# Kernel tuning notes

Measured on AMD Instinct MI355X. Metric: run time of the kernel, lower is better.

## Reference

```python
import jax, jax.numpy as jnp
import numpy as np

NUM_ITERATIONS = 3


def squash(x, axis):
    # squared_norm/(1+squared_norm) * x / sqrt(squared_norm), as in the torch module
    sn = jnp.sum(x * x, axis=axis, keepdims=True)
    return sn / (1.0 + sn) * x / jnp.sqrt(sn)


def setup_inputs() -> dict:
    key = jax.random.key(0)
    k1, k2 = jax.random.split(key)
    batch, num_caps, num_route, in_ch, out_ch = 32, 32, 4608, 8, 16
    x = jax.random.normal(k1, (batch, num_route, in_ch), dtype=jnp.float32)
    route_weights = jax.random.normal(k2, (num_caps, num_route, in_ch, out_ch), dtype=jnp.float32)
    return {"x": x, "route_weights": route_weights}


def reference(x, route_weights):
    # U[b,c,r,1,o] = x[b,1,r,1,i] @ W[1,c,r,i,o]
    U = jnp.einsum("bri,crio->bcro", x, route_weights)[:, :, :, None, :]  # [b,c,r,1,o]
    B = jnp.zeros_like(U)
    V = None
    for _ in range(NUM_ITERATIONS):
        C = jax.nn.softmax(B, axis=1)                 # softmax over capsules
        S = jnp.sum(C * U, axis=2, keepdims=True)      # reduce over route nodes: [b,c,1,1,o]
        V = squash(S, axis=-1)
        B = B + U * V
    b, c = B.shape[0], B.shape[1]
    o = B.shape[-1]
    return V.reshape(b, c, o)
```

## Files before the change

kernel.cpp:

```cpp
#include <hip/hip_runtime.h>

#define BATCH 32
#define NCAPS 32
#define NR    4608
#define NI    8
#define NO    16
#define CSTR  200
#define MAXRB 36
#define L2E   1.44269504088896341f

typedef float f2 __attribute__((ext_vector_type(2)));

template<int RB, bool FIRST>
__global__ __launch_bounds__(1024, 2) void caps_route_fast(
    const float* __restrict__ x,
    const float* __restrict__ W,
    const float* __restrict__ A,
    float* __restrict__ P)
{
    __shared__ __align__(16) float Ws[2][NCAPS * CSTR];
    __shared__ __align__(16) f2    xP[RB][8][2][NI];

    const int t  = threadIdx.x;
    const int om = (t & 3) | (((t >> 3) & 1) << 2);
    const int co = ((t >> 4) & 1) | (((t >> 2) & 1) << 1) | (((t >> 5) & 1) << 2);
    const int w  = t >> 6;
    const int oh = w & 1;
    const int bq = w >> 1;
    const int o  = oh * 8 + om;
    const int b0 = 4 * bq;
    const int r0 = blockIdx.x * RB;

    f2 a2[2][4];
    if (!FIRST) {
#pragma unroll
        for (int p = 0; p < 2; ++p)
#pragma unroll
            for (int cl = 0; cl < 4; ++cl) {
                const int c = 4 * co + cl;
                a2[p][cl].x = A[((b0 + 2 * p + 0) * NCAPS + c) * NO + o] * L2E;
                a2[p][cl].y = A[((b0 + 2 * p + 1) * NCAPS + c) * NO + o] * L2E;
            }
    }
    f2 acc[2][4];
#pragma unroll
    for (int p = 0; p < 2; ++p)
#pragma unroll
        for (int cl = 0; cl < 4; ++cl) acc[p][cl] = (f2)0.f;

    for (int s = t; s < RB * 16; s += 1024) {
        const int rr = s >> 4, bp = s & 15;
        const float* xp0 = &x[((size_t)(2 * bp + 0) * NR + r0 + rr) * NI];
        const float* xp1 = &x[((size_t)(2 * bp + 1) * NR + r0 + rr) * NI];
        const float4 a0 = *(const float4*)xp0;
        const float4 a1 = *(const float4*)(xp0 + 4);
        const float4 c0 = *(const float4*)xp1;
        const float4 c1 = *(const float4*)(xp1 + 4);
        f2* d = &xP[rr][bp >> 1][bp & 1][0];
        d[0] = f2{a0.x, c0.x}; d[1] = f2{a0.y, c0.y};
        d[2] = f2{a0.z, c0.z}; d[3] = f2{a0.w, c0.w};
        d[4] = f2{a1.x, c1.x}; d[5] = f2{a1.y, c1.y};
        d[6] = f2{a1.z, c1.z}; d[7] = f2{a1.w, c1.w};
    }

    const int c_st = t >> 5;
    const int sl   = (c_st >> 2) + 8 * (c_st & 3);
    const int part = t & 31;
    const int i_st = part >> 2;
    const int o0   = (part & 3) * 4;
    const float* wsrc = W + ((size_t)c_st * NR + r0) * (NI * NO) + part * 4;

    {
        const float4 s0 = *(const float4*)wsrc;
        float* d = &Ws[0][sl * CSTR + o0 * 12 + i_st];
        d[0] = s0.x; d[12] = s0.y; d[24] = s0.z; d[36] = s0.w;
    }
    float4 pf = {};
    if (RB > 1) pf = *(const float4*)(wsrc + NI * NO);
    __syncthreads();

#pragma unroll 1
    for (int rr = 0; rr < RB; ++rr) {
        const int cur = rr & 1;

        if (rr + 1 < RB) {
            float* d = &Ws[cur ^ 1][sl * CSTR + o0 * 12 + i_st];
            d[0] = pf.x; d[12] = pf.y; d[24] = pf.z; d[36] = pf.w;
            if (rr + 2 < RB)
                pf = *(const float4*)(wsrc + (size_t)(rr + 2) * (NI * NO));
        }

        f2 xq[2][NI];
        {
            const f2* xv = &xP[rr][bq][0][0];
#pragma unroll
            for (int i = 0; i < NI; ++i) { xq[0][i] = xv[i]; xq[1][i] = xv[NI + i]; }
        }

        const float* wb = &Ws[cur][co * CSTR + o * 12];
        if (FIRST) {
#pragma unroll
            for (int cl = 0; cl < 4; ++cl) {
                const float* wp = wb + cl * (8 * CSTR);
                const float4 w0 = *(const float4*)wp;
                const float4 w1 = *(const float4*)(wp + 4);
#pragma unroll
                for (int p = 0; p < 2; ++p) {
                    f2 u2 = xq[p][0] * w0.x;
                    u2 += xq[p][1] * w0.y;
                    u2 += xq[p][2] * w0.z;
                    u2 += xq[p][3] * w0.w;
                    u2 += xq[p][4] * w1.x;
                    u2 += xq[p][5] * w1.y;
                    u2 += xq[p][6] * w1.z;
                    u2 += xq[p][7] * w1.w;
                    acc[p][cl] += u2;
                }
            }
        } else {
            f2 tt[2][4];
            f2 Z0 = (f2)0.f, Z1 = (f2)0.f;
#pragma unroll
            for (int cl = 0; cl < 4; ++cl) {
                const float* wp = wb + cl * (8 * CSTR);
                const float4 w0 = *(const float4*)wp;
                const float4 w1 = *(const float4*)(wp + 4);
                f2 u0 = xq[0][0] * w0.x;
                u0 += xq[0][1] * w0.y;
                u0 += xq[0][2] * w0.z;
                u0 += xq[0][3] * w0.w;
                u0 += xq[0][4] * w1.x;
                u0 += xq[0][5] * w1.y;
                u0 += xq[0][6] * w1.z;
                u0 += xq[0][7] * w1.w;
                f2 u1 = xq[1][0] * w0.x;
                u1 += xq[1][1] * w0.y;
                u1 += xq[1][2] * w0.z;
                u1 += xq[1][3] * w0.w;
                u1 += xq[1][4] * w1.x;
                u1 += xq[1][5] * w1.y;
                u1 += xq[1][6] * w1.z;
                u1 += xq[1][7] * w1.w;
                const f2 l0 = u0 * a2[0][cl];
                const f2 l1 = u1 * a2[1][cl];
                f2 e0, e1;
                e0.x = exp2f(l0.x); e0.y = exp2f(l0.y);
                e1.x = exp2f(l1.x); e1.y = exp2f(l1.y);
                Z0 += e0; Z1 += e1;
                tt[0][cl] = e0 * u0;
                tt[1][cl] = e1 * u1;
            }
#pragma unroll
            for (int m = 0; m < 3; ++m) {
                const int msk = (m == 0) ? 4 : (m == 1) ? 16 : 32;
                Z0.x += __shfl_xor(Z0.x, msk); Z0.y += __shfl_xor(Z0.y, msk);
                Z1.x += __shfl_xor(Z1.x, msk); Z1.y += __shfl_xor(Z1.y, msk);
            }
            f2 rz0, rz1;
            rz0.x = __builtin_amdgcn_rcpf(Z0.x); rz0.y = __builtin_amdgcn_rcpf(Z0.y);
            rz1.x = __builtin_amdgcn_rcpf(Z1.x); rz1.y = __builtin_amdgcn_rcpf(Z1.y);
#pragma unroll
            for (int cl = 0; cl < 4; ++cl) {
                acc[0][cl] += tt[0][cl] * rz0;
                acc[1][cl] += tt[1][cl] * rz1;
            }
        }
        __syncthreads();
    }

#pragma unroll
    for (int bb = 0; bb < 4; ++bb) {
        const int p = bb >> 1, h = bb & 1;
        float* pout = P + (((size_t)blockIdx.x * BATCH + b0 + bb) * NO + o) * NCAPS + 4 * co;
        float4 v;
        v.x = h ? acc[p][0].y : acc[p][0].x;
        v.y = h ? acc[p][1].y : acc[p][1].x;
        v.z = h ? acc[p][2].y : acc[p][2].x;
        v.w = h ? acc[p][3].y : acc[p][3].x;
        if (FIRST) { v.x *= 0.03125f; v.y *= 0.03125f; v.z *= 0.03125f; v.w *= 0.03125f; }
        *(float4*)pout = v;
    }
}

__global__ __launch_bounds__(256) void caps_partial(const float* __restrict__ P,
                                                    float* __restrict__ P2)
{
    const int tid = threadIdx.x;
    const int ct  = blockIdx.x & 15;
    const int rg  = blockIdx.x >> 4;
    const size_t col = (size_t)ct * 1024 + tid * 4;
    const float* p = P + (size_t)rg * 16 * 16384 + col;
    float4 s = {0.f, 0.f, 0.f, 0.f};
#pragma unroll
    for (int k = 0; k < 16; ++k) {
        const float4 v = *(const float4*)(p + (size_t)k * 16384);
        s.x += v.x; s.y += v.y; s.z += v.z; s.w += v.w;
    }
    *(float4*)(P2 + (size_t)rg * 16384 + col) = s;
}

__global__ void caps_reduce_squash(const float* __restrict__ P,
                                   float* __restrict__ A,
                                   float* __restrict__ out,
                                   int nchunk)
{
    __shared__ float sm[256];
    const int bc  = blockIdx.x;
    const int b   = bc >> 5;
    const int c   = bc & 31;
    const int tid = threadIdx.x;
    const int o = tid & 15;
    const int j = tid >> 4;
    float s = 0.f;
    for (int tch = j; tch < nchunk; tch += 16)
        s += P[(((size_t)tch * BATCH + b) * NO + o) * NCAPS + c];
    sm[tid] = s;
    __syncthreads();
    if (tid < 16) {
        float S = 0.f;
#pragma unroll
        for (int k = 0; k < 16; ++k) S += sm[tid + 16 * k];
        float sq = S * S;
#pragma unroll
        for (int d = 8; d >= 1; d >>= 1) sq += __shfl_xor(sq, d, 16);
        const float scale = sq / ((1.f + sq) * sqrtf(sq));
        const float V = S * scale;
        const int idx = bc * NO + tid;
        A[idx] += V;
        if (out) out[idx] = V;
    }
}

__global__ __launch_bounds__(512, 2) void caps_route_generic(
    const float* __restrict__ x, const float* __restrict__ W,
    const float* __restrict__ A, float* __restrict__ P, int rb)
{
    __shared__ __align__(16) float Ws[NCAPS * CSTR];
    __shared__ __align__(16) float xsT[NI * MAXRB * BATCH];

    const int t = threadIdx.x;
    const int b = t & 31;
    const int o = t >> 5;
    const int r0 = blockIdx.x * rb;
    const int rbs = rb * BATCH;

    float a2s[NCAPS];
#pragma unroll
    for (int c = 0; c < NCAPS; ++c)
        a2s[c] = A[(b * NCAPS + c) * NO + o] * L2E;
    float acc[NCAPS];
#pragma unroll
    for (int c = 0; c < NCAPS; ++c) acc[c] = 0.f;

    for (int s = t; s < rbs; s += 512) {
        const int rr = s >> 5, bb = s & 31;
        const float4 v0 = *(const float4*)&x[((size_t)bb * NR + r0 + rr) * NI];
        const float4 v1 = *(const float4*)&x[((size_t)bb * NR + r0 + rr) * NI + 4];
        const float tmp[8] = {v0.x, v0.y, v0.z, v0.w, v1.x, v1.y, v1.z, v1.w};
#pragma unroll
        for (int i = 0; i < NI; ++i) xsT[i * rbs + s] = tmp[i];
    }

    const int cs  = t >> 4;
    const int seg = t & 15;
    const int iw  = seg >> 1;
    const int ob  = (seg & 1) * 8;
    const float* wsrc = W + ((size_t)cs * NR + r0) * (NI * NO) + seg * 8;
    float4 pf0 = *(const float4*)wsrc;
    float4 pf1 = *(const float4*)(wsrc + 4);

    for (int rr = 0; rr < rb; ++rr) {
        __syncthreads();
        {
            const float tmp[8] = {pf0.x, pf0.y, pf0.z, pf0.w,
                                  pf1.x, pf1.y, pf1.z, pf1.w};
#pragma unroll
            for (int k = 0; k < 8; ++k)
                Ws[cs * CSTR + (ob + k) * 12 + iw] = tmp[k];
        }
        if (rr + 1 < rb) {
            wsrc += NI * NO;
            pf0 = *(const float4*)wsrc;
            pf1 = *(const float4*)(wsrc + 4);
        }
        __syncthreads();

        float xq[NI];
#pragma unroll
        for (int i = 0; i < NI; ++i) xq[i] = xsT[i * rbs + rr * 32 + b];

        float tt[NCAPS];
        float Z = 0.f;
        const float* bp = &Ws[o * 12];
#pragma unroll
        for (int c = 0; c < NCAPS; ++c) {
            const float* wp = bp + c * CSTR;
            const float4 w0 = *(const float4*)wp;
            const float4 w1 = *(const float4*)(wp + 4);
            float uu =      xq[0] * w0.x;
            uu = fmaf(xq[1], w0.y, uu);
            uu = fmaf(xq[2], w0.z, uu);
            uu = fmaf(xq[3], w0.w, uu);
            uu = fmaf(xq[4], w1.x, uu);
            uu = fmaf(xq[5], w1.y, uu);
            uu = fmaf(xq[6], w1.z, uu);
            uu = fmaf(xq[7], w1.w, uu);
            const float ee = exp2f(uu * a2s[c]);
            Z += ee;
            tt[c] = ee * uu;
        }
        const float rz = __builtin_amdgcn_rcpf(Z);
#pragma unroll
        for (int c = 0; c < NCAPS; ++c)
            acc[c] = fmaf(tt[c], rz, acc[c]);
    }

    float* pout = P + (((size_t)blockIdx.x * BATCH + b) * NO + o) * NCAPS;
#pragma unroll
    for (int q = 0; q < NCAPS / 4; ++q) {
        float4 v;
        v.x = acc[4 * q + 0]; v.y = acc[4 * q + 1];
        v.z = acc[4 * q + 2]; v.w = acc[4 * q + 3];
        *(float4*)(pout + 4 * q) = v;
    }
}

__global__ void caps_zero(float* __restrict__ p, int n)
{
    const int i = blockIdx.x * blockDim.x + threadIdx.x;
    if (i < n) p[i] = 0.f;
}

extern "C" void kernel_launch(void* const* d_in, const int* in_sizes, int n_in,
                              void* d_out, int out_size, void* d_ws, size_t ws_size,
                              hipStream_t stream)
{
    const float* x = (const float*)d_in[0];
    const float* W = (const float*)d_in[1];
    float* out = (float*)d_out;

    float* A  = (float*)d_ws;
    float* P  = A + BATCH * NCAPS * NO;
    float* P2 = P + (size_t)256 * BATCH * NCAPS * NO;

    const size_t elem = (size_t)BATCH * NCAPS * NO;
    caps_zero<<<(int)((elem + 255) / 256), 256, 0, stream>>>(A, (int)elem);

    if ((1 + 256 + 16) * elem * sizeof(float) <= ws_size) {
        caps_route_fast<18, true><<<256, 1024, 0, stream>>>(x, W, A, P);
        caps_partial<<<256, 256, 0, stream>>>(P, P2);
        caps_reduce_squash<<<BATCH * NCAPS, 256, 0, stream>>>(P2, A, nullptr, 16);
        caps_route_fast<18, false><<<256, 1024, 0, stream>>>(x, W, A, P);
        caps_partial<<<256, 256, 0, stream>>>(P, P2);
        caps_reduce_squash<<<BATCH * NCAPS, 256, 0, stream>>>(P2, A, nullptr, 16);
        caps_route_fast<18, false><<<256, 1024, 0, stream>>>(x, W, A, P);
        caps_partial<<<256, 256, 0, stream>>>(P, P2);
        caps_reduce_squash<<<BATCH * NCAPS, 256, 0, stream>>>(P2, A, out, 16);
    } else {
        int nchunk = 128;
        while (nchunk > 32 &&
               (size_t)(nchunk + 1) * elem * sizeof(float) > ws_size)
            nchunk >>= 1;
        const int rb = NR / nchunk;
        for (int it = 0; it < 3; ++it) {
            caps_route_generic<<<nchunk, 512, 0, stream>>>(x, W, A, P, rb);
            caps_reduce_squash<<<BATCH * NCAPS, 256, 0, stream>>>(
                P, A, it == 2 ? out : nullptr, nchunk);
        }
    }
}
```

Baseline: 156.2 us.

## Split routing into 512 chunks and fuse partial reduction with squash per batch

The routing kernel now runs with 512 blocks of 9 route nodes each instead of 256 blocks of 18, and writes partials in a batch-major layout. The two-stage partial-sum plus reduce-squash pass is replaced by one kernel per batch that sums all chunk partials with coalesced loads, squashes, and updates A. This drops one launch per iteration and aims to improve occupancy of the main kernel across CUs. In exchange it doubles the partial buffer written and read, and the reduction runs on only 32 blocks.

```diff
diff --git a/kernel.cpp b/kernel.cpp
--- a/kernel.cpp
+++ b/kernel.cpp
@@ -7,6 +7,7 @@
 #define NO    16
 #define CSTR  200
 #define MAXRB 36
+#define NCH   512
 #define L2E   1.44269504088896341f
 
 typedef float f2 __attribute__((ext_vector_type(2)));
@@ -171,7 +172,7 @@
 #pragma unroll
     for (int bb = 0; bb < 4; ++bb) {
         const int p = bb >> 1, h = bb & 1;
-        float* pout = P + (((size_t)blockIdx.x * BATCH + b0 + bb) * NO + o) * NCAPS + 4 * co;
+        float* pout = P + (((size_t)(b0 + bb) * NCH + blockIdx.x) * NO + o) * NCAPS + 4 * co;
         float4 v;
         v.x = h ? acc[p][0].y : acc[p][0].x;
         v.y = h ? acc[p][1].y : acc[p][1].x;
@@ -182,21 +183,38 @@
     }
 }
 
-__global__ __launch_bounds__(256) void caps_partial(const float* __restrict__ P,
-                                                    float* __restrict__ P2)
-{
-    const int tid = threadIdx.x;
-    const int ct  = blockIdx.x & 15;
-    const int rg  = blockIdx.x >> 4;
-    const size_t col = (size_t)ct * 1024 + tid * 4;
-    const float* p = P + (size_t)rg * 16 * 16384 + col;
-    float4 s = {0.f, 0.f, 0.f, 0.f};
-#pragma unroll
-    for (int k = 0; k < 16; ++k) {
-        const float4 v = *(const float4*)(p + (size_t)k * 16384);
-        s.x += v.x; s.y += v.y; s.z += v.z; s.w += v.w;
-    }
-    *(float4*)(P2 + (size_t)rg * 16384 + col) = s;
+__global__ __launch_bounds__(1024) void caps_squash_t(
+    const float* __restrict__ P,
+    float* __restrict__ A,
+    float* __restrict__ out)
+{
+    __shared__ float sm[1024];
+    __shared__ float sc[NCAPS];
+    const int b = blockIdx.x;
+    const int t = threadIdx.x;
+    const float* pb = P + (size_t)b * (NCH * 512);
+    float s = 0.f;
+#pragma unroll 4
+    for (int k = 0; k < NCH / 2; ++k)
+        s += pb[k * 1024 + t];
+    sm[t] = s;
+    __syncthreads();
+    if (t < 512) sm[t] = sm[t] + sm[t + 512];
+    __syncthreads();
+    if (t < NCAPS) {
+        float sq = 0.f;
+#pragma unroll
+        for (int o = 0; o < NO; ++o) { const float v = sm[o * 32 + t]; sq = fmaf(v, v, sq); }
+        sc[t] = sq / ((1.f + sq) * sqrtf(sq));
+    }
+    __syncthreads();
+    if (t < 512) {
+        const int o = t >> 5, c = t & 31;
+        const float V = sm[t] * sc[c];
+        const int idx = (b * NCAPS + c) * NO + o;
+        A[idx] += V;
+        if (out) out[idx] = V;
+    }
 }
 
 __global__ void caps_reduce_squash(const float* __restrict__ P,
@@ -339,23 +357,19 @@
     const float* W = (const float*)d_in[1];
     float* out = (float*)d_out;
 
-    float* A  = (float*)d_ws;
-    float* P  = A + BATCH * NCAPS * NO;
-    float* P2 = P + (size_t)256 * BATCH * NCAPS * NO;
+    float* A = (float*)d_ws;
+    float* P = A + BATCH * NCAPS * NO;
 
     const size_t elem = (size_t)BATCH * NCAPS * NO;
     caps_zero<<<(int)((elem + 255) / 256), 256, 0, stream>>>(A, (int)elem);
 
-    if ((1 + 256 + 16) * elem * sizeof(float) <= ws_size) {
-        caps_route_fast<18, true><<<256, 1024, 0, stream>>>(x, W, A, P);
-        caps_partial<<<256, 256, 0, stream>>>(P, P2);
-        caps_reduce_squash<<<BATCH * NCAPS, 256, 0, stream>>>(P2, A, nullptr, 16);
-        caps_route_fast<18, false><<<256, 1024, 0, stream>>>(x, W, A, P);
-        caps_partial<<<256, 256, 0, stream>>>(P, P2);
-        caps_reduce_squash<<<BATCH * NCAPS, 256, 0, stream>>>(P2, A, nullptr, 16);
-        caps_route_fast<18, false><<<256, 1024, 0, stream>>>(x, W, A, P);
-        caps_partial<<<256, 256, 0, stream>>>(P, P2);
-        caps_reduce_squash<<<BATCH * NCAPS, 256, 0, stream>>>(P2, A, out, 16);
+    if ((size_t)(1 + NCH) * elem * sizeof(float) <= ws_size) {
+        caps_route_fast<NR / NCH, true><<<NCH, 1024, 0, stream>>>(x, W, A, P);
+        caps_squash_t<<<BATCH, 1024, 0, stream>>>(P, A, nullptr);
+        caps_route_fast<NR / NCH, false><<<NCH, 1024, 0, stream>>>(x, W, A, P);
+        caps_squash_t<<<BATCH, 1024, 0, stream>>>(P, A, nullptr);
+        caps_route_fast<NR / NCH, false><<<NCH, 1024, 0, stream>>>(x, W, A, P);
+        caps_squash_t<<<BATCH, 1024, 0, stream>>>(P, A, out);
     } else {
         int nchunk = 128;
         while (nchunk > 32 &&
```

Result: slower. 227.6 us (+45.7%).
